# Kernel tuning notes

Measured on AMD Instinct MI355X. Metric: run time of the kernel, lower is better.

The kernel has to match this reference:

```python
import jax, jax.numpy as jnp
import numpy as np

ALPHA = 0.5  # matches init_kwargs alpha
EPS = 1e-6
NUM_CLASSES = 100000
FEAT_DIM = 256
BATCH = 16384


def setup_inputs() -> dict:
    key = jax.random.key(0)
    k1, k2, k3 = jax.random.split(key, 3)
    centers = jax.random.normal(k1, (NUM_CLASSES, FEAT_DIM), dtype=jnp.float32)
    features = jax.random.normal(k2, (BATCH, FEAT_DIM), dtype=jnp.float32)
    target = jax.random.randint(k3, (BATCH,), 0, NUM_CLASSES, dtype=jnp.int64)
    return {"centers": centers, "features": features, "target": target}


def reference(centers, features, target):
    # Gather centers for each sample's label: [B, D]
    centers_batch = centers[target]
    # MSE loss (mean over all elements), same as nn.MSELoss()
    center_loss = jnp.mean(jnp.square(features - centers_batch))
    # Per-sample residual
    diff = centers_batch - features  # [B, D]
    # appear_times[i] = number of samples in batch sharing target[i]
    counts = jnp.zeros((centers.shape[0],), dtype=centers.dtype).at[target].add(1.0)
    appear_times = counts[target][:, None]  # [B, 1]
    # Normalized, scaled update (torch code divides by count + eps, scales by alpha)
    update = (ALPHA * diff) / (appear_times + EPS)
    # Serial loop `centers[target[i]] -= update[i]` == scatter-subtract with accumulation
    new_centers = centers.at[target].add(-update)
    return center_loss, new_centers
```

## Files before the change

kernel.cpp:

```cpp
#include <hip/hip_runtime.h>

#define NUM_CLASSES 100000
#define FEAT_DIM    256
#define BATCH       16384
#define ALPHA       0.5f
#define EPS_        1e-6f

typedef float f4 __attribute__((ext_vector_type(4)));

#define OFF_COUNTS    0u
#define OFF_HEAD      400000u
#define OFF_NSLOTS    800000u
#define OFF_ZERO_END  800016u
#define OFF_SLOT      OFF_ZERO_END
#define OFF_NEXT      (OFF_SLOT + 400000u)
#define OFF_PART2     (OFF_NEXT + 65536u)

__global__ void zero_kernel(f4* __restrict__ p, int n) {
    int i = blockIdx.x * blockDim.x + threadIdx.x;
    if (i < n) p[i] = (f4){0.f, 0.f, 0.f, 0.f};
}

__global__ void count_slot_kernel(const int* __restrict__ target,
                                  int* __restrict__ counts,
                                  int* __restrict__ head,
                                  int* __restrict__ next,
                                  int* __restrict__ slot_of,
                                  int* __restrict__ nslots) {
    int i = blockIdx.x * blockDim.x + threadIdx.x;
    if (i < BATCH) {
        int t = target[i];
        int old = atomicAdd(&counts[t], 1);
        if (old == 0) slot_of[t] = atomicAdd(nslots, 1);
        int prev = atomicExch(&head[t], i + 1);
        next[i] = prev;
    }
}

__global__ void rewrite_kernel(const float* __restrict__ centers,
                               const float* __restrict__ features,
                               const int*   __restrict__ counts,
                               const int*   __restrict__ head,
                               const int*   __restrict__ next,
                               const int*   __restrict__ slot_of,
                               float*       __restrict__ out_centers,
                               float*       __restrict__ partials2) {
    const int wave = threadIdx.x >> 6;
    const int lane = threadIdx.x & 63;
    const int row = blockIdx.x * 4 + wave;
    if (row >= NUM_CLASSES) return;

    const size_t base = (size_t)row * FEAT_DIM + lane;
    const float* crow = centers + base;
    float*       orow = out_centers + base;

    const float c0 = crow[0], c1 = crow[64], c2 = crow[128], c3 = crow[192];
    const int cnt = counts[row];

    if (cnt == 0) {
        orow[0]   = c0;
        orow[64]  = c1;
        orow[128] = c2;
        orow[192] = c3;
        return;
    }

    float s0 = 0.f, s1 = 0.f, s2 = 0.f, s3 = 0.f, sq = 0.f;
    for (int j = head[row]; j != 0; j = next[j - 1]) {
        const float* frow = features + (size_t)(j - 1) * FEAT_DIM + lane;
        const float f0 = frow[0], f1 = frow[64], f2 = frow[128], f3 = frow[192];
        s0 += f0; s1 += f1; s2 += f2; s3 += f3;
        sq += f0*f0 + f1*f1 + f2*f2 + f3*f3;
    }

    const float fc  = (float)cnt;
    const float inv = ALPHA / (fc + EPS_);
    orow[0]   = c0 - inv * (fc * c0 - s0);
    orow[64]  = c1 - inv * (fc * c1 - s1);
    orow[128] = c2 - inv * (fc * c2 - s2);
    orow[192] = c3 - inv * (fc * c3 - s3);

    float red = sq
              + fc * (c0*c0 + c1*c1 + c2*c2 + c3*c3)
              - 2.0f * (c0*s0 + c1*s1 + c2*s2 + c3*s3);
    #pragma unroll
    for (int off = 32; off > 0; off >>= 1)
        red += __shfl_down(red, off, 64);
    if (lane == 0) partials2[slot_of[row]] = red;
}

__global__ void reduce_loss(const float* __restrict__ partials2,
                            const int*   __restrict__ nslots,
                            float* __restrict__ out) {
    const int ns = *nslots;
    float s = 0.0f;
    for (int i = threadIdx.x; i < ns; i += 1024) s += partials2[i];
    #pragma unroll
    for (int off = 32; off > 0; off >>= 1)
        s += __shfl_down(s, off, 64);
    __shared__ float wsum[16];
    const int lane = threadIdx.x & 63;
    const int wid  = threadIdx.x >> 6;
    if (lane == 0) wsum[wid] = s;
    __syncthreads();
    if (threadIdx.x == 0) {
        float tot = 0.0f;
        #pragma unroll
        for (int k = 0; k < 16; ++k) tot += wsum[k];
        out[0] = tot * (1.0f / ((float)BATCH * (float)FEAT_DIM));
    }
}

extern "C" void kernel_launch(void* const* d_in, const int* in_sizes, int n_in,
                              void* d_out, int out_size, void* d_ws, size_t ws_size,
                              hipStream_t stream) {
    const float* centers  = (const float*)d_in[0];
    const float* features = (const float*)d_in[1];
    const int*   target   = (const int*)d_in[2];

    float* out         = (float*)d_out;
    float* out_centers = out + 1;

    char* ws = (char*)d_ws;
    int*   counts    = (int*)(ws + OFF_COUNTS);
    int*   head      = (int*)(ws + OFF_HEAD);
    int*   nslots    = (int*)(ws + OFF_NSLOTS);
    int*   slot_of   = (int*)(ws + OFF_SLOT);
    int*   next      = (int*)(ws + OFF_NEXT);
    float* partials2 = (float*)(ws + OFF_PART2);

    const int nzero = (int)(OFF_ZERO_END / 16u);
    zero_kernel<<<(nzero + 255) / 256, 256, 0, stream>>>((f4*)ws, nzero);

    count_slot_kernel<<<(BATCH + 255) / 256, 256, 0, stream>>>(target, counts, head, next,
                                                               slot_of, nslots);

    rewrite_kernel<<<NUM_CLASSES / 4, 256, 0, stream>>>(centers, features, counts, head,
                                                        next, slot_of, out_centers, partials2);

    reduce_loss<<<1, 1024, 0, stream>>>(partials2, nslots, out);
}
```

Before: 55.85 us.

## Drop slot compaction, use per-row partials with multi-block reduction, nontemporal stores

```diff
diff --git a/kernel.cpp b/kernel.cpp
--- a/kernel.cpp
+++ b/kernel.cpp
@@ -10,45 +10,40 @@
 
 #define OFF_COUNTS    0u
 #define OFF_HEAD      400000u
-#define OFF_NSLOTS    800000u
-#define OFF_ZERO_END  800016u
-#define OFF_SLOT      OFF_ZERO_END
-#define OFF_NEXT      (OFF_SLOT + 400000u)
-#define OFF_PART2     (OFF_NEXT + 65536u)
+#define OFF_PARTW     800000u
+#define OFF_DONE      1200000u
+#define OFF_ZERO_END  1200016u
+#define OFF_NEXT      OFF_ZERO_END
+#define OFF_PART64    (OFF_NEXT + 65536u)
 
 __global__ void zero_kernel(f4* __restrict__ p, int n) {
     int i = blockIdx.x * blockDim.x + threadIdx.x;
     if (i < n) p[i] = (f4){0.f, 0.f, 0.f, 0.f};
 }
 
-__global__ void count_slot_kernel(const int* __restrict__ target,
-                                  int* __restrict__ counts,
-                                  int* __restrict__ head,
-                                  int* __restrict__ next,
-                                  int* __restrict__ slot_of,
-                                  int* __restrict__ nslots) {
+__global__ void count_kernel(const int* __restrict__ target,
+                             int* __restrict__ counts,
+                             int* __restrict__ head,
+                             int* __restrict__ next) {
     int i = blockIdx.x * blockDim.x + threadIdx.x;
     if (i < BATCH) {
         int t = target[i];
-        int old = atomicAdd(&counts[t], 1);
-        if (old == 0) slot_of[t] = atomicAdd(nslots, 1);
+        atomicAdd(&counts[t], 1);
         int prev = atomicExch(&head[t], i + 1);
         next[i] = prev;
     }
 }
 
-__global__ void rewrite_kernel(const float* __restrict__ centers,
+__global__ __launch_bounds__(256) void rewrite_kernel(
+                               const float* __restrict__ centers,
                                const float* __restrict__ features,
                                const int*   __restrict__ counts,
                                const int*   __restrict__ head,
                                const int*   __restrict__ next,
-                               const int*   __restrict__ slot_of,
                                float*       __restrict__ out_centers,
-                               float*       __restrict__ partials2) {
-    const int wave = threadIdx.x >> 6;
+                               float*       __restrict__ partw) {
     const int lane = threadIdx.x & 63;
-    const int row = blockIdx.x * 4 + wave;
-    if (row >= NUM_CLASSES) return;
+    const int row  = blockIdx.x * 4 + (threadIdx.x >> 6);
 
     const size_t base = (size_t)row * FEAT_DIM + lane;
     const float* crow = centers + base;
@@ -58,10 +53,10 @@
     const int cnt = counts[row];
 
     if (cnt == 0) {
-        orow[0]   = c0;
-        orow[64]  = c1;
-        orow[128] = c2;
-        orow[192] = c3;
+        __builtin_nontemporal_store(c0, orow);
+        __builtin_nontemporal_store(c1, orow + 64);
+        __builtin_nontemporal_store(c2, orow + 128);
+        __builtin_nontemporal_store(c3, orow + 192);
         return;
     }
 
@@ -75,10 +70,10 @@
 
     const float fc  = (float)cnt;
     const float inv = ALPHA / (fc + EPS_);
-    orow[0]   = c0 - inv * (fc * c0 - s0);
-    orow[64]  = c1 - inv * (fc * c1 - s1);
-    orow[128] = c2 - inv * (fc * c2 - s2);
-    orow[192] = c3 - inv * (fc * c3 - s3);
+    __builtin_nontemporal_store(c0 - inv * (fc * c0 - s0), orow);
+    __builtin_nontemporal_store(c1 - inv * (fc * c1 - s1), orow + 64);
+    __builtin_nontemporal_store(c2 - inv * (fc * c2 - s2), orow + 128);
+    __builtin_nontemporal_store(c3 - inv * (fc * c3 - s3), orow + 192);
 
     float red = sq
               + fc * (c0*c0 + c1*c1 + c2*c2 + c3*c3)
@@ -86,28 +81,35 @@
     #pragma unroll
     for (int off = 32; off > 0; off >>= 1)
         red += __shfl_down(red, off, 64);
-    if (lane == 0) partials2[slot_of[row]] = red;
+    if (lane == 0) partw[row] = red;
 }
 
-__global__ void reduce_loss(const float* __restrict__ partials2,
-                            const int*   __restrict__ nslots,
-                            float* __restrict__ out) {
-    const int ns = *nslots;
-    float s = 0.0f;
-    for (int i = threadIdx.x; i < ns; i += 1024) s += partials2[i];
+__global__ void reduce_fin(const float* __restrict__ partw,
+                           float* __restrict__ part64,
+                           int*   __restrict__ done,
+                           float* __restrict__ out) {
+    float s = 0.f;
+    for (int i = blockIdx.x * 256 + threadIdx.x; i < NUM_CLASSES; i += 64 * 256)
+        s += partw[i];
     #pragma unroll
     for (int off = 32; off > 0; off >>= 1)
         s += __shfl_down(s, off, 64);
-    __shared__ float wsum[16];
+    __shared__ float wsum[4];
     const int lane = threadIdx.x & 63;
     const int wid  = threadIdx.x >> 6;
     if (lane == 0) wsum[wid] = s;
     __syncthreads();
     if (threadIdx.x == 0) {
-        float tot = 0.0f;
-        #pragma unroll
-        for (int k = 0; k < 16; ++k) tot += wsum[k];
-        out[0] = tot * (1.0f / ((float)BATCH * (float)FEAT_DIM));
+        part64[blockIdx.x] = wsum[0] + wsum[1] + wsum[2] + wsum[3];
+        __threadfence();
+        int old = atomicAdd(done, 1);
+        if (old == 63) {
+            __threadfence();
+            float acc = 0.f;
+            #pragma unroll
+            for (int k = 0; k < 64; ++k) acc += part64[k];
+            out[0] = acc * (1.0f / ((float)BATCH * (float)FEAT_DIM));
+        }
     }
 }
 
@@ -122,21 +124,20 @@
     float* out_centers = out + 1;
 
     char* ws = (char*)d_ws;
-    int*   counts    = (int*)(ws + OFF_COUNTS);
-    int*   head      = (int*)(ws + OFF_HEAD);
-    int*   nslots    = (int*)(ws + OFF_NSLOTS);
-    int*   slot_of   = (int*)(ws + OFF_SLOT);
-    int*   next      = (int*)(ws + OFF_NEXT);
-    float* partials2 = (float*)(ws + OFF_PART2);
+    int*   counts  = (int*)(ws + OFF_COUNTS);
+    int*   head    = (int*)(ws + OFF_HEAD);
+    float* partw   = (float*)(ws + OFF_PARTW);
+    int*   done    = (int*)(ws + OFF_DONE);
+    int*   next    = (int*)(ws + OFF_NEXT);
+    float* part64  = (float*)(ws + OFF_PART64);
 
     const int nzero = (int)(OFF_ZERO_END / 16u);
     zero_kernel<<<(nzero + 255) / 256, 256, 0, stream>>>((f4*)ws, nzero);
 
-    count_slot_kernel<<<(BATCH + 255) / 256, 256, 0, stream>>>(target, counts, head, next,
-                                                               slot_of, nslots);
+    count_kernel<<<(BATCH + 255) / 256, 256, 0, stream>>>(target, counts, head, next);
 
     rewrite_kernel<<<NUM_CLASSES / 4, 256, 0, stream>>>(centers, features, counts, head,
-                                                        next, slot_of, out_centers, partials2);
+                                                        next, out_centers, partw);
 
-    reduce_loss<<<1, 1024, 0, stream>>>(partials2, nslots, out);
+    reduce_fin<<<64, 256, 0, stream>>>(partw, part64, done, out);
 }
```

Result: faster. 53.33 us (median of 2 runs) (-4.5%).

## Split center update into bulk vectorized copy plus sparse touched-row fix kernel

Applied to the files above, without the earlier changes.

```diff
diff --git a/kernel.cpp b/kernel.cpp
--- a/kernel.cpp
+++ b/kernel.cpp
@@ -7,13 +7,16 @@
 #define EPS_        1e-6f
 
 typedef float f4 __attribute__((ext_vector_type(4)));
+typedef f4 __attribute__((aligned(4))) f4_u;
+
+#define NQ (NUM_CLASSES * FEAT_DIM / 4)
 
 #define OFF_COUNTS    0u
 #define OFF_HEAD      400000u
 #define OFF_NSLOTS    800000u
 #define OFF_ZERO_END  800016u
-#define OFF_SLOT      OFF_ZERO_END
-#define OFF_NEXT      (OFF_SLOT + 400000u)
+#define OFF_TOUCHED   OFF_ZERO_END
+#define OFF_NEXT      (OFF_TOUCHED + 65536u)
 #define OFF_PART2     (OFF_NEXT + 65536u)
 
 __global__ void zero_kernel(f4* __restrict__ p, int n) {
@@ -21,49 +24,54 @@
     if (i < n) p[i] = (f4){0.f, 0.f, 0.f, 0.f};
 }
 
-__global__ void count_slot_kernel(const int* __restrict__ target,
-                                  int* __restrict__ counts,
-                                  int* __restrict__ head,
-                                  int* __restrict__ next,
-                                  int* __restrict__ slot_of,
-                                  int* __restrict__ nslots) {
+__global__ void count_kernel(const int* __restrict__ target,
+                             int* __restrict__ counts,
+                             int* __restrict__ head,
+                             int* __restrict__ next,
+                             int* __restrict__ touched,
+                             int* __restrict__ nslots) {
     int i = blockIdx.x * blockDim.x + threadIdx.x;
     if (i < BATCH) {
         int t = target[i];
         int old = atomicAdd(&counts[t], 1);
-        if (old == 0) slot_of[t] = atomicAdd(nslots, 1);
+        if (old == 0) {
+            int s = atomicAdd(nslots, 1);
+            touched[s] = t;
+        }
         int prev = atomicExch(&head[t], i + 1);
         next[i] = prev;
     }
 }
 
-__global__ void rewrite_kernel(const float* __restrict__ centers,
+__global__ __launch_bounds__(256) void copy_kernel(const float* __restrict__ centers,
+                                                   float* __restrict__ out) {
+    const int stride = gridDim.x * blockDim.x;
+    for (int q = 1 + blockIdx.x * blockDim.x + threadIdx.x; q < NQ; q += stride) {
+        const f4 v = *(const f4_u*)(centers + 4 * (size_t)q - 1);
+        __builtin_nontemporal_store(v, (f4*)(out + 4 * (size_t)q));
+    }
+}
+
+__global__ __launch_bounds__(256) void fix_kernel(
+                               const float* __restrict__ centers,
                                const float* __restrict__ features,
                                const int*   __restrict__ counts,
                                const int*   __restrict__ head,
                                const int*   __restrict__ next,
-                               const int*   __restrict__ slot_of,
+                               const int*   __restrict__ touched,
+                               const int*   __restrict__ nslots,
                                float*       __restrict__ out_centers,
                                float*       __restrict__ partials2) {
-    const int wave = threadIdx.x >> 6;
     const int lane = threadIdx.x & 63;
-    const int row = blockIdx.x * 4 + wave;
-    if (row >= NUM_CLASSES) return;
+    const int slot = blockIdx.x * 4 + (threadIdx.x >> 6);
+    if (slot >= *nslots) return;
+    const int row = touched[slot];
 
     const size_t base = (size_t)row * FEAT_DIM + lane;
     const float* crow = centers + base;
     float*       orow = out_centers + base;
-
     const float c0 = crow[0], c1 = crow[64], c2 = crow[128], c3 = crow[192];
     const int cnt = counts[row];
-
-    if (cnt == 0) {
-        orow[0]   = c0;
-        orow[64]  = c1;
-        orow[128] = c2;
-        orow[192] = c3;
-        return;
-    }
 
     float s0 = 0.f, s1 = 0.f, s2 = 0.f, s3 = 0.f, sq = 0.f;
     for (int j = head[row]; j != 0; j = next[j - 1]) {
@@ -86,12 +94,14 @@
     #pragma unroll
     for (int off = 32; off > 0; off >>= 1)
         red += __shfl_down(red, off, 64);
-    if (lane == 0) partials2[slot_of[row]] = red;
+    if (lane == 0) partials2[slot] = red;
 }
 
-__global__ void reduce_loss(const float* __restrict__ partials2,
-                            const int*   __restrict__ nslots,
-                            float* __restrict__ out) {
+__global__ void reduce_fin(const float* __restrict__ partials2,
+                           const int*   __restrict__ nslots,
+                           const int*   __restrict__ counts,
+                           const float* __restrict__ centers,
+                           float* __restrict__ out) {
     const int ns = *nslots;
     float s = 0.0f;
     for (int i = threadIdx.x; i < ns; i += 1024) s += partials2[i];
@@ -108,6 +118,12 @@
         #pragma unroll
         for (int k = 0; k < 16; ++k) tot += wsum[k];
         out[0] = tot * (1.0f / ((float)BATCH * (float)FEAT_DIM));
+        if (counts[0] == 0) {
+            out[1] = centers[0]; out[2] = centers[1]; out[3] = centers[2];
+        }
+        if (counts[NUM_CLASSES - 1] == 0) {
+            out[(size_t)NQ * 4] = centers[(size_t)NQ * 4 - 1];
+        }
     }
 }
 
@@ -125,18 +141,20 @@
     int*   counts    = (int*)(ws + OFF_COUNTS);
     int*   head      = (int*)(ws + OFF_HEAD);
     int*   nslots    = (int*)(ws + OFF_NSLOTS);
-    int*   slot_of   = (int*)(ws + OFF_SLOT);
+    int*   touched   = (int*)(ws + OFF_TOUCHED);
     int*   next      = (int*)(ws + OFF_NEXT);
     float* partials2 = (float*)(ws + OFF_PART2);
 
     const int nzero = (int)(OFF_ZERO_END / 16u);
     zero_kernel<<<(nzero + 255) / 256, 256, 0, stream>>>((f4*)ws, nzero);
 
-    count_slot_kernel<<<(BATCH + 255) / 256, 256, 0, stream>>>(target, counts, head, next,
-                                                               slot_of, nslots);
+    count_kernel<<<(BATCH + 255) / 256, 256, 0, stream>>>(target, counts, head, next,
+                                                          touched, nslots);
 
-    rewrite_kernel<<<NUM_CLASSES / 4, 256, 0, stream>>>(centers, features, counts, head,
-                                                        next, slot_of, out_centers, partials2);
+    copy_kernel<<<12800, 256, 0, stream>>>(centers, out);
 
-    reduce_loss<<<1, 1024, 0, stream>>>(partials2, nslots, out);
+    fix_kernel<<<BATCH / 4, 256, 0, stream>>>(centers, features, counts, head, next,
+                                              touched, nslots, out_centers, partials2);
+
+    reduce_fin<<<1, 1024, 0, stream>>>(partials2, nslots, counts, centers, out);
 }
```

Result: slower. 63.37 us (+13.4%).
